# Kernel tuning notes

Hardware: AMD Instinct MI355X
Metric: run time of the kernel (lower is better)

## Reference

```python
import jax, jax.numpy as jnp
import numpy as np

B, S, D, P, NQ = 8, 2048, 1024, 256, 8192


def setup_inputs() -> dict:
    key = jax.random.key(0)
    ks = jax.random.split(key, 8)
    return {
        "flag": 0,
        "encoded_input": jax.random.normal(ks[0], (B, S, D), dtype=jnp.float32),
        "start_ids_1": jax.random.randint(ks[1], (NQ,), 0, S, dtype=jnp.int32),
        "end_ids_1": jax.random.randint(ks[2], (NQ,), 0, S, dtype=jnp.int32),
        "query_batch_idx": jax.random.randint(ks[3], (NQ,), 0, B, dtype=jnp.int32),
        "start_ids_2": jax.random.randint(ks[4], (NQ,), 0, S, dtype=jnp.int32),
        "end_ids_2": jax.random.randint(ks[5], (NQ,), 0, S, dtype=jnp.int32),
        "W": jax.random.normal(ks[6], (D, P), dtype=jnp.float32) * 0.02,
        "b": jnp.zeros((P,), dtype=jnp.float32),
    }


def _gather_spans(h, qb, s, e):
    # span_repr[b, i, j] = concat(h[b, i], h[b, j]) for j >= i, else 0.
    # Direct gather instead of building the O(seq^2) table.
    rep = jnp.concatenate([h[qb, s], h[qb, e]], axis=-1)  # [NQ, 2*P]
    valid = (e >= s).astype(rep.dtype)[:, None]
    return rep * valid


def reference(flag, encoded_input, start_ids_1, end_ids_1, query_batch_idx,
              start_ids_2, end_ids_2, W, b):
    h = encoded_input @ W + b  # [B, S, P] (use_proj=True)
    res1 = _gather_spans(h, query_batch_idx, start_ids_1, end_ids_1)
    res2 = _gather_spans(h, query_batch_idx, start_ids_2, end_ids_2)
    return (res1, res2)
```

## Files before the change

### kernel.cpp

```cpp
#include <hip/hip_runtime.h>
#include <hip/hip_bf16.h>
#include <stdint.h>

#define S_LEN 2048
#define D_DIM 1024
#define P_DIM 256
#define NQ_   8192
#define M_TOT 16384

#define BM 32
#define BN 256
#define BK 64

typedef __attribute__((ext_vector_type(4))) float  f32x4;
typedef __attribute__((ext_vector_type(8))) __bf16 bf16x8;
typedef __attribute__((ext_vector_type(4))) __bf16 bf16x4;

__device__ __forceinline__ void async16(const void* g, void* l) {
    __builtin_amdgcn_global_load_lds(
        (const __attribute__((address_space(1))) uint32_t*)g,
        (__attribute__((address_space(3))) uint32_t*)l, 16, 0, 0);
}

__device__ __forceinline__ void nts(f32x4 v, float* p) {
    __builtin_nontemporal_store(v, (f32x4*)p);
}

__global__ __launch_bounds__(1024) void wt_kernel(const float* __restrict__ W,
                                                  __bf16* __restrict__ WT) {
    __shared__ __bf16 tile[32][33];
    const int k0 = blockIdx.x * 32;
    const int n0 = blockIdx.y * 32;
    const int tx = threadIdx.x, ty = threadIdx.y;
    tile[ty][tx] = (__bf16)W[(k0 + ty) * P_DIM + (n0 + tx)];
    __syncthreads();
    WT[(n0 + ty) * D_DIM + (k0 + tx)] = tile[tx][ty];
}

__global__ __launch_bounds__(256, 2) void gemm_kernel(const float*  __restrict__ A,
                                                      const __bf16* __restrict__ WT,
                                                      const float*  __restrict__ bias,
                                                      __bf16*       __restrict__ H) {
    __shared__ __bf16 Bs[2][BN * BK];

    const int tid = threadIdx.x;
    const int w   = tid >> 6;
    const int l   = tid & 63;
    const int lm  = l & 15;
    const int q   = l >> 4;

    const int m0 = blockIdx.x * BM;

    const int brow_l = l >> 3;
    const int bc     = (l & 7) ^ (brow_l & 7);

    auto stageB = [&](int buf, int k0) {
        #pragma unroll
        for (int j = 0; j < 8; ++j) {
            const int r   = w * 8 + j;
            const int row = r * 8 + brow_l;
            async16(WT + (size_t)row * D_DIM + k0 + bc * 8, &Bs[buf][r * 512]);
        }
    };

    const float* ap0 = A + (size_t)(m0 + lm)      * D_DIM + q * 8;
    const float* ap1 = A + (size_t)(m0 + 16 + lm) * D_DIM + q * 8;

    f32x4 acc[2][4] = {};
    float4 ra0[2][2][2];
    float4 ra1[2][2][2];

    auto loadA = [&](float4 (&ra)[2][2][2], int k0) {
        #pragma unroll
        for (int kh = 0; kh < 2; ++kh) {
            ra[0][kh][0] = *(const float4*)(ap0 + k0 + kh * 32);
            ra[0][kh][1] = *(const float4*)(ap0 + k0 + kh * 32 + 4);
            ra[1][kh][0] = *(const float4*)(ap1 + k0 + kh * 32);
            ra[1][kh][1] = *(const float4*)(ap1 + k0 + kh * 32 + 4);
        }
    };

    auto compute = [&](const float4 (&ra)[2][2][2], int buf) {
        #pragma unroll
        for (int kh = 0; kh < 2; ++kh) {
            const int pos = ((kh * 4 + q) ^ (lm & 7)) * 8;
            bf16x8 bfr[4];
            #pragma unroll
            for (int ni = 0; ni < 4; ++ni)
                bfr[ni] = *(const bf16x8*)(&Bs[buf][(w * 64 + ni * 16 + lm) * BK + pos]);
            bf16x8 af[2];
            #pragma unroll
            for (int mi = 0; mi < 2; ++mi) {
                af[mi][0] = (__bf16)ra[mi][kh][0].x; af[mi][1] = (__bf16)ra[mi][kh][0].y;
                af[mi][2] = (__bf16)ra[mi][kh][0].z; af[mi][3] = (__bf16)ra[mi][kh][0].w;
                af[mi][4] = (__bf16)ra[mi][kh][1].x; af[mi][5] = (__bf16)ra[mi][kh][1].y;
                af[mi][6] = (__bf16)ra[mi][kh][1].z; af[mi][7] = (__bf16)ra[mi][kh][1].w;
            }
            #pragma unroll
            for (int mi = 0; mi < 2; ++mi)
                #pragma unroll
                for (int ni = 0; ni < 4; ++ni)
                    acc[mi][ni] = __builtin_amdgcn_mfma_f32_16x16x32_bf16(
                        af[mi], bfr[ni], acc[mi][ni], 0, 0, 0);
        }
    };

    loadA(ra0, 0);
    stageB(0, 0);
    __syncthreads();

    #pragma unroll 1
    for (int ph = 0; ph < 7; ++ph) {
        const int k1 = (2 * ph + 1) * BK, k2 = (2 * ph + 2) * BK;
        loadA(ra1, k1); stageB(1, k1);
        __builtin_amdgcn_sched_barrier(0);
        compute(ra0, 0);
        __syncthreads();
        loadA(ra0, k2); stageB(0, k2);
        __builtin_amdgcn_sched_barrier(0);
        compute(ra1, 1);
        __syncthreads();
    }
    loadA(ra1, 15 * BK); stageB(1, 15 * BK);
    __builtin_amdgcn_sched_barrier(0);
    compute(ra0, 0);
    __syncthreads();
    compute(ra1, 1);

    #pragma unroll
    for (int ni = 0; ni < 4; ++ni) {
        const int col = w * 64 + ni * 16 + lm;
        const float bv = bias[col];
        #pragma unroll
        for (int mi = 0; mi < 2; ++mi) {
            const int rbase = m0 + mi * 16 + q * 4;
            #pragma unroll
            for (int r = 0; r < 4; ++r)
                H[(size_t)(rbase + r) * P_DIM + col] = (__bf16)(acc[mi][ni][r] + bv);
        }
    }
}

__global__ __launch_bounds__(256) void gather_kernel(const __bf16* __restrict__ H,
                                                     const int* __restrict__ s1,
                                                     const int* __restrict__ e1,
                                                     const int* __restrict__ qb,
                                                     const int* __restrict__ s2,
                                                     const int* __restrict__ e2,
                                                     float* __restrict__ out) {
    const int wave = (blockIdx.x * 256 + threadIdx.x) >> 6;
    const int l    = threadIdx.x & 63;

    #pragma unroll
    for (int j = 0; j < 8; ++j) {
        const int p   = wave * 8 + j;
        const int set = p >> 13;
        const int qi  = p & 8191;
        const int s   = set ? s2[qi] : s1[qi];
        const int e   = set ? e2[qi] : e1[qi];
        const int b   = qb[qi];

        f32x4 v0 = {0.f, 0.f, 0.f, 0.f}, v1 = v0;
        if (e >= s) {
            const bf16x4 a = *(const bf16x4*)(H + ((size_t)b * S_LEN + s) * P_DIM + l * 4);
            const bf16x4 c = *(const bf16x4*)(H + ((size_t)b * S_LEN + e) * P_DIM + l * 4);
            v0[0] = (float)a[0]; v0[1] = (float)a[1]; v0[2] = (float)a[2]; v0[3] = (float)a[3];
            v1[0] = (float)c[0]; v1[1] = (float)c[1]; v1[2] = (float)c[2]; v1[3] = (float)c[3];
        }
        float* op = out + (size_t)set * (NQ_ * 512) + (size_t)qi * 512;
        nts(v0, op + l * 4);
        nts(v1, op + 256 + l * 4);
    }
}

extern "C" void kernel_launch(void* const* d_in, const int* in_sizes, int n_in,
                              void* d_out, int out_size, void* d_ws, size_t ws_size,
                              hipStream_t stream) {
    const float* A    = (const float*)d_in[1];
    const int*   s1   = (const int*)  d_in[2];
    const int*   e1   = (const int*)  d_in[3];
    const int*   qb   = (const int*)  d_in[4];
    const int*   s2   = (const int*)  d_in[5];
    const int*   e2   = (const int*)  d_in[6];
    const float* W    = (const float*)d_in[7];
    const float* bias = (const float*)d_in[8];
    float*       out  = (float*)d_out;

    __bf16* WT = (__bf16*)d_ws;
    __bf16* H  = (__bf16*)((char*)d_ws + (1 << 20));

    wt_kernel    <<<dim3(32, 8), dim3(32, 32), 0, stream>>>(W, WT);
    gemm_kernel  <<<dim3(M_TOT / BM), dim3(256), 0, stream>>>(A, WT, bias, H);
    gather_kernel<<<dim3(512), dim3(256), 0, stream>>>(H, s1, e1, qb, s2, e2, out);
}
```

Measured before the change: 163.8 us.

## Stage A tile through LDS as bf16 and halve BK for higher occupancy

The GEMM kernel no longer has each wave load its own fp32 A rows into registers and convert them there. Half the threads now load the A tile once, convert it to bf16 and write it to a padded shared buffer that all four waves read. BK drops from 64 to 32 with a new rotation swizzle for B, and launch bounds move from 2 to 4 blocks per CU, which cuts LDS and register use per block to allow more resident waves. The cost is twice as many k-iterations and barriers, plus an extra LDS write and read round-trip for A.

```diff
diff --git a/kernel.cpp b/kernel.cpp
--- a/kernel.cpp
+++ b/kernel.cpp
@@ -10,7 +10,8 @@
 
 #define BM 32
 #define BN 256
-#define BK 64
+#define BK 32
+#define ASTRIDE 40
 
 typedef __attribute__((ext_vector_type(4))) float  f32x4;
 typedef __attribute__((ext_vector_type(8))) __bf16 bf16x8;
@@ -37,10 +38,11 @@
     WT[(n0 + ty) * D_DIM + (k0 + tx)] = tile[tx][ty];
 }
 
-__global__ __launch_bounds__(256, 2) void gemm_kernel(const float*  __restrict__ A,
+__global__ __launch_bounds__(256, 4) void gemm_kernel(const float*  __restrict__ A,
                                                       const __bf16* __restrict__ WT,
                                                       const float*  __restrict__ bias,
                                                       __bf16*       __restrict__ H) {
+    __shared__ __bf16 As[2][BM * ASTRIDE];
     __shared__ __bf16 Bs[2][BN * BK];
 
     const int tid = threadIdx.x;
@@ -51,81 +53,86 @@
 
     const int m0 = blockIdx.x * BM;
 
-    const int brow_l = l >> 3;
-    const int bc     = (l & 7) ^ (brow_l & 7);
+    const int bi  = l >> 2;
+    const int bqf = ((l & 3) - (l >> 3)) & 3;
 
     auto stageB = [&](int buf, int k0) {
         #pragma unroll
-        for (int j = 0; j < 8; ++j) {
-            const int r   = w * 8 + j;
-            const int row = r * 8 + brow_l;
-            async16(WT + (size_t)row * D_DIM + k0 + bc * 8, &Bs[buf][r * 512]);
-        }
-    };
-
-    const float* ap0 = A + (size_t)(m0 + lm)      * D_DIM + q * 8;
-    const float* ap1 = A + (size_t)(m0 + 16 + lm) * D_DIM + q * 8;
+        for (int j = 0; j < 4; ++j) {
+            const int g   = w * 4 + j;
+            const int row = g * 16 + bi;
+            async16(WT + (size_t)row * D_DIM + k0 + bqf * 8, &Bs[buf][g * 512]);
+        }
+    };
+
+    const int ar = tid >> 2;
+    const int ac = tid & 3;
+    const float* agp = A + (size_t)(m0 + ar) * D_DIM + ac * 8;
+
+    float4 fa0, fa1;
+    auto loadA = [&](int k0) {
+        if (tid < 128) {
+            fa0 = *(const float4*)(agp + k0);
+            fa1 = *(const float4*)(agp + k0 + 4);
+        }
+    };
+    auto writeA = [&](int buf) {
+        if (tid < 128) {
+            bf16x8 v;
+            v[0] = (__bf16)fa0.x; v[1] = (__bf16)fa0.y; v[2] = (__bf16)fa0.z; v[3] = (__bf16)fa0.w;
+            v[4] = (__bf16)fa1.x; v[5] = (__bf16)fa1.y; v[6] = (__bf16)fa1.z; v[7] = (__bf16)fa1.w;
+            *(bf16x8*)(&As[buf][ar * ASTRIDE + ac * 8]) = v;
+        }
+    };
 
     f32x4 acc[2][4] = {};
-    float4 ra0[2][2][2];
-    float4 ra1[2][2][2];
-
-    auto loadA = [&](float4 (&ra)[2][2][2], int k0) {
-        #pragma unroll
-        for (int kh = 0; kh < 2; ++kh) {
-            ra[0][kh][0] = *(const float4*)(ap0 + k0 + kh * 32);
-            ra[0][kh][1] = *(const float4*)(ap0 + k0 + kh * 32 + 4);
-            ra[1][kh][0] = *(const float4*)(ap1 + k0 + kh * 32);
-            ra[1][kh][1] = *(const float4*)(ap1 + k0 + kh * 32 + 4);
-        }
-    };
-
-    auto compute = [&](const float4 (&ra)[2][2][2], int buf) {
-        #pragma unroll
-        for (int kh = 0; kh < 2; ++kh) {
-            const int pos = ((kh * 4 + q) ^ (lm & 7)) * 8;
-            bf16x8 bfr[4];
+
+    auto compute = [&](int buf) {
+        bf16x8 af[2], bfr[4];
+        #pragma unroll
+        for (int mi = 0; mi < 2; ++mi)
+            af[mi] = *(const bf16x8*)(&As[buf][(mi * 16 + lm) * ASTRIDE + q * 8]);
+        #pragma unroll
+        for (int ni = 0; ni < 4; ++ni) {
+            const int g = w * 4 + ni;
+            bfr[ni] = *(const bf16x8*)(&Bs[buf][g * 512 + lm * 32 + ((q + (lm >> 1)) & 3) * 8]);
+        }
+        #pragma unroll
+        for (int mi = 0; mi < 2; ++mi)
             #pragma unroll
             for (int ni = 0; ni < 4; ++ni)
-                bfr[ni] = *(const bf16x8*)(&Bs[buf][(w * 64 + ni * 16 + lm) * BK + pos]);
-            bf16x8 af[2];
-            #pragma unroll
-            for (int mi = 0; mi < 2; ++mi) {
-                af[mi][0] = (__bf16)ra[mi][kh][0].x; af[mi][1] = (__bf16)ra[mi][kh][0].y;
-                af[mi][2] = (__bf16)ra[mi][kh][0].z; af[mi][3] = (__bf16)ra[mi][kh][0].w;
-                af[mi][4] = (__bf16)ra[mi][kh][1].x; af[mi][5] = (__bf16)ra[mi][kh][1].y;
-                af[mi][6] = (__bf16)ra[mi][kh][1].z; af[mi][7] = (__bf16)ra[mi][kh][1].w;
-            }
-            #pragma unroll
-            for (int mi = 0; mi < 2; ++mi)
-                #pragma unroll
-                for (int ni = 0; ni < 4; ++ni)
-                    acc[mi][ni] = __builtin_amdgcn_mfma_f32_16x16x32_bf16(
-                        af[mi], bfr[ni], acc[mi][ni], 0, 0, 0);
-        }
-    };
-
-    loadA(ra0, 0);
+                acc[mi][ni] = __builtin_amdgcn_mfma_f32_16x16x32_bf16(
+                    af[mi], bfr[ni], acc[mi][ni], 0, 0, 0);
+    };
+
+    loadA(0);
     stageB(0, 0);
+    writeA(0);
     __syncthreads();
 
     #pragma unroll 1
-    for (int ph = 0; ph < 7; ++ph) {
+    for (int ph = 0; ph < 15; ++ph) {
         const int k1 = (2 * ph + 1) * BK, k2 = (2 * ph + 2) * BK;
-        loadA(ra1, k1); stageB(1, k1);
-        __builtin_amdgcn_sched_barrier(0);
-        compute(ra0, 0);
+        loadA(k1); stageB(1, k1);
+        __builtin_amdgcn_sched_barrier(0);
+        compute(0);
+        __builtin_amdgcn_sched_barrier(0);
+        writeA(1);
         __syncthreads();
-        loadA(ra0, k2); stageB(0, k2);
-        __builtin_amdgcn_sched_barrier(0);
-        compute(ra1, 1);
+        loadA(k2); stageB(0, k2);
+        __builtin_amdgcn_sched_barrier(0);
+        compute(1);
+        __builtin_amdgcn_sched_barrier(0);
+        writeA(0);
         __syncthreads();
     }
-    loadA(ra1, 15 * BK); stageB(1, 15 * BK);
+    loadA(31 * BK); stageB(1, 31 * BK);
     __builtin_amdgcn_sched_barrier(0);
-    compute(ra0, 0);
+    compute(0);
+    __builtin_amdgcn_sched_barrier(0);
+    writeA(1);
     __syncthreads();
-    compute(ra1, 1);
+    compute(1);
 
     #pragma unroll
     for (int ni = 0; ni < 4; ++ni) {
```

New measurement: 152.2 us. -7.1%, faster.

## Stage A tile through LDS and read weights directly from global memory

Applied to the files above, without the earlier changes.

The GEMM's operand roles are swapped. The fp32 activation tile A is now staged asynchronously into LDS with an XOR swizzle, while the bf16 transposed weights are loaded straight from global (L2-resident) into registers each k-step. The aim is to cut LDS footprint and the large per-block B staging traffic, since every block re-staged the full 256x64 weight slice. In exchange, each wave issues uncoalesced-ish global weight loads directly before compute, which may expose latency because only the A tile is double-buffered.

```diff
diff --git a/kernel.cpp b/kernel.cpp
--- a/kernel.cpp
+++ b/kernel.cpp
@@ -41,7 +41,7 @@
                                                       const __bf16* __restrict__ WT,
                                                       const float*  __restrict__ bias,
                                                       __bf16*       __restrict__ H) {
-    __shared__ __bf16 Bs[2][BN * BK];
+    __shared__ float As[2][BM * BK];
 
     const int tid = threadIdx.x;
     const int w   = tid >> 6;
@@ -51,81 +51,64 @@
 
     const int m0 = blockIdx.x * BM;
 
-    const int brow_l = l >> 3;
-    const int bc     = (l & 7) ^ (brow_l & 7);
-
-    auto stageB = [&](int buf, int k0) {
+    auto stageA = [&](int buf, int k0) {
         #pragma unroll
-        for (int j = 0; j < 8; ++j) {
-            const int r   = w * 8 + j;
-            const int row = r * 8 + brow_l;
-            async16(WT + (size_t)row * D_DIM + k0 + bc * 8, &Bs[buf][r * 512]);
+        for (int jj = 0; jj < 2; ++jj) {
+            const int j = 2 * w + jj;
+            const int r = 4 * j + (l >> 4);
+            const int c = (l & 15) ^ (r & 15);
+            async16(A + (size_t)(m0 + r) * D_DIM + k0 + c * 4,
+                    &As[buf][j * 256]);
         }
     };
 
-    const float* ap0 = A + (size_t)(m0 + lm)      * D_DIM + q * 8;
-    const float* ap1 = A + (size_t)(m0 + 16 + lm) * D_DIM + q * 8;
+    f32x4 acc[2][4] = {};
 
-    f32x4 acc[2][4] = {};
-    float4 ra0[2][2][2];
-    float4 ra1[2][2][2];
+    const __bf16* wp = WT + (size_t)(w * 64 + lm) * D_DIM + q * 8;
 
-    auto loadA = [&](float4 (&ra)[2][2][2], int k0) {
+    auto step = [&](int buf, int k0, int kstage) {
+        bf16x8 rb[2][4];
+        #pragma unroll
+        for (int kh = 0; kh < 2; ++kh)
+            #pragma unroll
+            for (int ni = 0; ni < 4; ++ni)
+                rb[kh][ni] = *(const bf16x8*)(wp + (size_t)ni * 16 * D_DIM + k0 + kh * 32);
+        if (kstage >= 0) stageA(buf ^ 1, kstage);
+        __builtin_amdgcn_sched_barrier(0);
         #pragma unroll
         for (int kh = 0; kh < 2; ++kh) {
-            ra[0][kh][0] = *(const float4*)(ap0 + k0 + kh * 32);
-            ra[0][kh][1] = *(const float4*)(ap0 + k0 + kh * 32 + 4);
-            ra[1][kh][0] = *(const float4*)(ap1 + k0 + kh * 32);
-            ra[1][kh][1] = *(const float4*)(ap1 + k0 + kh * 32 + 4);
-        }
-    };
-
-    auto compute = [&](const float4 (&ra)[2][2][2], int buf) {
-        #pragma unroll
-        for (int kh = 0; kh < 2; ++kh) {
-            const int pos = ((kh * 4 + q) ^ (lm & 7)) * 8;
-            bf16x8 bfr[4];
-            #pragma unroll
-            for (int ni = 0; ni < 4; ++ni)
-                bfr[ni] = *(const bf16x8*)(&Bs[buf][(w * 64 + ni * 16 + lm) * BK + pos]);
             bf16x8 af[2];
             #pragma unroll
             for (int mi = 0; mi < 2; ++mi) {
-                af[mi][0] = (__bf16)ra[mi][kh][0].x; af[mi][1] = (__bf16)ra[mi][kh][0].y;
-                af[mi][2] = (__bf16)ra[mi][kh][0].z; af[mi][3] = (__bf16)ra[mi][kh][0].w;
-                af[mi][4] = (__bf16)ra[mi][kh][1].x; af[mi][5] = (__bf16)ra[mi][kh][1].y;
-                af[mi][6] = (__bf16)ra[mi][kh][1].z; af[mi][7] = (__bf16)ra[mi][kh][1].w;
+                const int row = mi * 16 + lm;
+                const int c0  = kh * 8 + q * 2;
+                const f32x4 a0 = *(const f32x4*)(&As[buf][row * BK + ((c0 ^ lm) * 4)]);
+                const f32x4 a1 = *(const f32x4*)(&As[buf][row * BK + (((c0 + 1) ^ lm) * 4)]);
+                af[mi][0] = (__bf16)a0[0]; af[mi][1] = (__bf16)a0[1];
+                af[mi][2] = (__bf16)a0[2]; af[mi][3] = (__bf16)a0[3];
+                af[mi][4] = (__bf16)a1[0]; af[mi][5] = (__bf16)a1[1];
+                af[mi][6] = (__bf16)a1[2]; af[mi][7] = (__bf16)a1[3];
             }
             #pragma unroll
             for (int mi = 0; mi < 2; ++mi)
                 #pragma unroll
                 for (int ni = 0; ni < 4; ++ni)
                     acc[mi][ni] = __builtin_amdgcn_mfma_f32_16x16x32_bf16(
-                        af[mi], bfr[ni], acc[mi][ni], 0, 0, 0);
+                        af[mi], rb[kh][ni], acc[mi][ni], 0, 0, 0);
         }
+        __syncthreads();
     };
 
-    loadA(ra0, 0);
-    stageB(0, 0);
+    stageA(0, 0);
     __syncthreads();
 
     #pragma unroll 1
     for (int ph = 0; ph < 7; ++ph) {
-        const int k1 = (2 * ph + 1) * BK, k2 = (2 * ph + 2) * BK;
-        loadA(ra1, k1); stageB(1, k1);
-        __builtin_amdgcn_sched_barrier(0);
-        compute(ra0, 0);
-        __syncthreads();
-        loadA(ra0, k2); stageB(0, k2);
-        __builtin_amdgcn_sched_barrier(0);
-        compute(ra1, 1);
-        __syncthreads();
+        step(0, (2 * ph) * BK,     (2 * ph + 1) * BK);
+        step(1, (2 * ph + 1) * BK, (2 * ph + 2) * BK);
     }
-    loadA(ra1, 15 * BK); stageB(1, 15 * BK);
-    __builtin_amdgcn_sched_barrier(0);
-    compute(ra0, 0);
-    __syncthreads();
-    compute(ra1, 1);
+    step(0, 14 * BK, 15 * BK);
+    step(1, 15 * BK, -1);
 
     #pragma unroll
     for (int ni = 0; ni < 4; ++ni) {
```

Measured after the change: 149.9 us. 1.09x faster.
